# Performance work log

Measured on AMD Instinct MI355X. Metric: run time of the kernel, lower is better.

Reference implementation:

```python
import jax, jax.numpy as jnp
import numpy as np

WS = 8   # window_size
SS = 4   # shift_size
NH = 6   # num_heads
EPS = 1e-5


def _win_partition(x, ws):
    # x: [B, H, W, C] -> [B * H/ws * W/ws, ws*ws, C]
    B, H, W, C = x.shape
    x = x.reshape(B, H // ws, ws, W // ws, ws, C)
    return x.transpose(0, 1, 3, 2, 4, 5).reshape(-1, ws * ws, C)


def _win_reverse(wins, ws, H, W, B):
    C = wins.shape[-1]
    x = wins.reshape(B, H // ws, W // ws, ws, ws, C)
    return x.transpose(0, 1, 3, 2, 4, 5).reshape(B, H, W, C)


def _rel_pos_index(ws):
    # static numpy computation, identical to the torch buffer
    coords = np.stack(np.meshgrid(np.arange(ws), np.arange(ws), indexing='ij')).reshape(2, -1)
    rel = coords[:, :, None] - coords[:, None, :]          # [2, N, N]
    rel = rel.transpose(1, 2, 0).copy()                    # [N, N, 2]
    rel[..., 0] += ws - 1
    rel[..., 1] += ws - 1
    rel[..., 0] *= 2 * ws - 1
    return rel.sum(-1)                                     # [N, N] int


def _attn_mask_np(H, W, ws, ss):
    # static numpy computation of the SW-MSA mask, identical to _compute_mask
    img = np.zeros((1, H, W, 1), np.float32)
    cnt = 0
    for hs in (slice(0, -ws), slice(-ws, -ss), slice(-ss, None)):
        for wsl in (slice(0, -ws), slice(-ws, -ss), slice(-ss, None)):
            img[:, hs, wsl, :] = cnt
            cnt += 1
    mw = img.reshape(1, H // ws, ws, W // ws, ws, 1).transpose(0, 1, 3, 2, 4, 5).reshape(-1, ws * ws)
    am = mw[:, None, :] - mw[:, :, None]                   # [nW, N, N]
    return np.where(am != 0, np.float32(-100.0), np.float32(0.0))


def _swin_forward(x, qkv_w, qkv_b, proj_w, proj_b, rpb_table,
                  norm2_g, norm2_b, mlp_w1, mlp_b1, mlp_w2, mlp_b2, H, W):
    B, L, C = x.shape
    ws, ss, nh = WS, SS, NH
    hd = C // nh
    x2d = x.reshape(B, H, W, C)
    shifted = jnp.roll(x2d, (-ss, -ss), axis=(1, 2))
    win = _win_partition(shifted, ws)                      # [B_, N, C]
    B_, N, _ = win.shape

    # --- window attention (note: original applies attention to un-normalized x) ---
    qkv = (win @ qkv_w + qkv_b).reshape(B_, N, 3, nh, hd)
    q = qkv[:, :, 0].transpose(0, 2, 1, 3)                 # [B_, nh, N, hd]
    k = qkv[:, :, 1].transpose(0, 2, 1, 3)
    v = qkv[:, :, 2].transpose(0, 2, 1, 3)
    attn = jnp.einsum('bhnd,bhmd->bhnm', q, k) * (hd ** -0.5)

    bias = rpb_table[jnp.asarray(_rel_pos_index(ws)).reshape(-1)]
    bias = bias.reshape(N, N, nh).transpose(2, 0, 1)       # [nh, N, N]
    attn = attn + bias[None]

    mask = jnp.asarray(_attn_mask_np(H, W, ws, ss))        # [nW, N, N]
    nW = mask.shape[0]
    attn = attn.reshape(B_ // nW, nW, nh, N, N) + mask[None, :, None]
    attn = jax.nn.softmax(attn.reshape(B_, nh, N, N), axis=-1)

    out = jnp.einsum('bhnm,bhmd->bnhd', attn, v).reshape(B_, N, C)
    out = out @ proj_w + proj_b

    x2d = _win_reverse(out, ws, H, W, B)
    x2d = jnp.roll(x2d, (ss, ss), axis=(1, 2))
    x = x + x2d.reshape(B, L, C)

    # --- MLP branch with LayerNorm (norm2) ---
    mu = x.mean(-1, keepdims=True)
    var = x.var(-1, keepdims=True)
    xn = (x - mu) * jax.lax.rsqrt(var + EPS) * norm2_g + norm2_b
    h = jax.nn.gelu(xn @ mlp_w1 + mlp_b1, approximate=False)
    return x + (h @ mlp_w2 + mlp_b2)


def setup_inputs() -> dict:
    B, H, W, C = 8, 128, 128, 192
    mlp_hidden = 4 * C
    ks = jax.random.split(jax.random.key(0), 6)
    std = 0.02
    return {
        'x': jax.random.normal(ks[0], (B, H * W, C), jnp.float32),
        'qkv_w': jax.random.normal(ks[1], (C, 3 * C), jnp.float32) * std,
        'qkv_b': jnp.zeros((3 * C,), jnp.float32),
        'proj_w': jax.random.normal(ks[2], (C, C), jnp.float32) * std,
        'proj_b': jnp.zeros((C,), jnp.float32),
        'rpb_table': jax.random.normal(ks[3], ((2 * WS - 1) ** 2, NH), jnp.float32) * std,
        'norm2_g': jnp.ones((C,), jnp.float32),
        'norm2_b': jnp.zeros((C,), jnp.float32),
        'mlp_w1': jax.random.normal(ks[4], (C, mlp_hidden), jnp.float32) * std,
        'mlp_b1': jnp.zeros((mlp_hidden,), jnp.float32),
        'mlp_w2': jax.random.normal(ks[5], (mlp_hidden, C), jnp.float32) * std,
        'mlp_b2': jnp.zeros((C,), jnp.float32),
        'H': H,
        'W': W,
    }


def reference(x, qkv_w, qkv_b, proj_w, proj_b, rpb_table, norm2_g, norm2_b,
              mlp_w1, mlp_b1, mlp_w2, mlp_b2, H, W):
    return _swin_forward(x, qkv_w, qkv_b, proj_w, proj_b, rpb_table,
                         norm2_g, norm2_b, mlp_w1, mlp_b1, mlp_w2, mlp_b2, H, W)
```

## Files before the change

kernel.cpp:

```cpp
#include <hip/hip_runtime.h>
#include <hip/hip_bf16.h>


typedef __hip_bfloat16 bf16;
typedef __attribute__((ext_vector_type(8))) short bfrag;
typedef __attribute__((ext_vector_type(4))) float ffrag;

union bfu { bf16 h[8]; bfrag v; };

__device__ __forceinline__ float b2f(bf16 v) { return __bfloat162float(v); }
__device__ __forceinline__ bf16  f2b(float v) { return __float2bfloat16(v); }

#define MFMA(a, b, c) __builtin_amdgcn_mfma_f32_16x16x32_bf16((a), (b), (c), 0, 0, 0)

#define WS_XRES  0ULL
#define WS_OG    100663296ULL
#define WS_QKVTG 150994944ULL
#define WS_QBG   151250944ULL
#define WS_PROJT 151253504ULL
#define WS_W1T   151330304ULL
#define WS_W2T   151637504ULL
#define WS_SB    152006144ULL

__device__ __forceinline__ void stage_lds(const void* g, void* l, int nbytes, int t) {
    const int lane16 = (t & 63) * 16;
    for (int base = (t >> 6) * 1024; base < nbytes; base += 4096) {
        if (base + lane16 < nbytes) {
            __builtin_amdgcn_global_load_lds(
                (const __attribute__((address_space(1))) void*)((const char*)g + base + lane16),
                (__attribute__((address_space(3))) void*)((char*)l + base),
                16, 0, 0);
        }
    }
}

__device__ __forceinline__ float gelu_t(float x) {
    float y = x * (1.5957691216057308f + 0.07135481627f * x * x);
    return x * (1.f / (1.f + __expf(-y)));
}

__global__ __launch_bounds__(256) void k_prep(
    const float* __restrict__ qkv_w, const float* __restrict__ qkv_b,
    const float* __restrict__ proj_w, const float* __restrict__ w1,
    const float* __restrict__ w2, const float* __restrict__ rpb,
    char* __restrict__ ws)
{
    int i = blockIdx.x * 256 + threadIdx.x;
    bf16*  qkvTg = (bf16*)(ws + WS_QKVTG);
    float* qbg   = (float*)(ws + WS_QBG);
    bf16*  projT = (bf16*)(ws + WS_PROJT);
    bf16*  w1T   = (bf16*)(ws + WS_W1T);
    bf16*  w2T   = (bf16*)(ws + WS_W2T);
    bf16*  sbB   = (bf16*)(ws + WS_SB);

    if (i < 128000) {
        int g = i / 64000, rem = i % 64000;
        int c = rem / 200, k = rem % 200;
        float v = 0.f;
        if (k < 192) {
            if (c < 96)       v = qkv_w[k * 576 + g * 96 + c];
            else if (c < 192) v = qkv_w[k * 576 + 192 + g * 96 + (c - 96)];
            else if (c < 288) v = qkv_w[k * 576 + 384 + g * 96 + (c - 192)];
        }
        qkvTg[i] = f2b(v);
    } else if (i < 128640) {
        int j = i - 128000;
        int g = j / 320, c = j % 320;
        float v = 0.f;
        if (c < 96)       v = qkv_b[g * 96 + c];
        else if (c < 192) v = qkv_b[192 + g * 96 + (c - 96)];
        else if (c < 288) v = qkv_b[384 + g * 96 + (c - 192)];
        qbg[j] = v;
    } else if (i < 167040) {
        int j = i - 128640;
        int c = j / 200, k = j % 200;
        projT[j] = f2b(k < 192 ? proj_w[k * 192 + c] : 0.f);
    } else if (i < 320640) {
        int j = i - 167040;
        int c = j / 200, k = j % 200;
        w1T[j] = f2b(k < 192 ? w1[k * 768 + c] : 0.f);
    } else if (i < 504960) {
        int j = i - 320640;
        int kc = j / 7680, r = (j % 7680) / 40, kk = j % 40;
        w2T[j] = f2b(kk < 32 ? w2[(kc * 32 + kk) * 192 + r] : 0.f);
    } else if (i < 603264) {
        int j = i - 504960;
        int cls = j / 24576, h = (j % 24576) / 4096;
        int ii = (j % 4096) / 64, jj = j % 64;
        int ri = ii >> 3, ci = ii & 7, rj = jj >> 3, cj = jj & 7;
        float bias = rpb[(((ri - rj + 7) * 15) + (ci - cj + 7)) * 6 + h];
        int clsR = cls >> 1, clsC = cls & 1;
        int regi = (clsR ? (ri < 4 ? 1 : 2) : 0) * 3 + (clsC ? (ci < 4 ? 1 : 2) : 0);
        int regj = (clsR ? (rj < 4 ? 1 : 2) : 0) * 3 + (clsC ? (cj < 4 ? 1 : 2) : 0);
        sbB[j] = f2b(bias + (regi == regj ? 0.f : -100.f));
    }
}

__global__ __launch_bounds__(256, 2) void k_attn(
    const float* __restrict__ x, const char* __restrict__ ws,
    bf16* __restrict__ Og)
{
    __shared__ __align__(16) unsigned char smem[77824];
    bf16*  sWb = (bf16*)(smem);
    bf16*  sQ  = (bf16*)(smem + 25600);
    bf16*  sK  = (bf16*)(smem + 38912);
    bf16*  sVT = (bf16*)(smem + 52224);
    bf16*  sP  = (bf16*)(smem + 66048);
    float* sQB = (float*)(smem + 75264);

    const bf16*  qkvTg = (const bf16*)(ws + WS_QKVTG);
    const float* qbg   = (const float*)(ws + WS_QBG);
    const bf16*  sbB   = (const bf16*)(ws + WS_SB);

    const int t    = threadIdx.x;
    const int lane = t & 63, quad = lane >> 4, l15 = lane & 15;
    const int wave = t >> 6, r0 = wave * 16;
    const int win = blockIdx.x;
    const int b   = win >> 8;
    const int wi  = win & 255;
    const int wh  = wi >> 4, wwi = wi & 15;

    stage_lds(qbg, smem + 75264, 2560, t);
    stage_lds(qkvTg, sWb, 12800, t);

    bfrag aX[6];
    {
        int row = r0 + l15;
        int rr = row >> 3, cc = row & 7;
        int hs  = (wh * 8 + rr + 4) & 127;
        int wsx = (wwi * 8 + cc + 4) & 127;
        const float* xrow = x + ((size_t)(b * 16384 + hs * 128 + wsx)) * 192;
        #pragma unroll
        for (int kb = 0; kb < 6; kb++) {
            float4 f0 = *(const float4*)(xrow + kb * 32 + quad * 8);
            float4 f1 = *(const float4*)(xrow + kb * 32 + quad * 8 + 4);
            bfu u;
            u.h[0] = f2b(f0.x); u.h[1] = f2b(f0.y); u.h[2] = f2b(f0.z); u.h[3] = f2b(f0.w);
            u.h[4] = f2b(f1.x); u.h[5] = f2b(f1.y); u.h[6] = f2b(f1.z); u.h[7] = f2b(f1.w);
            aX[kb] = u.v;
        }
    }

    const int cls = ((wh == 15) ? 2 : 0) + ((wwi == 15) ? 1 : 0);
    const bf16* bBc = sbB + (size_t)cls * 24576;
    bf16* sPw = sP + wave * 16 * 72;

    __syncthreads();

    int pb = 0;
    for (int g = 0; g < 2; g++) {
        for (int c = 0; c < 9; c++) {
            if (c < 8)
                stage_lds(qkvTg + (size_t)(g * 320 + (c + 1) * 32) * 200,
                          sWb + (pb ^ 1) * 6400, 12800, t);
            else if (g == 0)
                stage_lds(qkvTg + (size_t)320 * 200,
                          sWb + (pb ^ 1) * 6400, 12800, t);
            const bf16* sW = sWb + pb * 6400;
            #pragma unroll
            for (int ct = 0; ct < 2; ct++) {
                int c0 = c * 32 + ct * 16;
                bfrag bw[6];
                #pragma unroll
                for (int kb = 0; kb < 6; kb++)
                    bw[kb] = *(const bfrag*)&sW[(ct * 16 + l15) * 200 + kb * 32 + quad * 8];
                ffrag acc = {0.f, 0.f, 0.f, 0.f};
                #pragma unroll
                for (int kb = 0; kb < 6; kb++) acc = MFMA(aX[kb], bw[kb], acc);
                float bias = sQB[g * 320 + c0 + l15];
                #pragma unroll
                for (int reg = 0; reg < 4; reg++) {
                    int r = r0 + quad * 4 + reg;
                    float v = acc[reg] + bias;
                    if (c0 < 96)       sQ[r * 104 + c0 + l15] = f2b(v);
                    else if (c0 < 192) sK[r * 104 + (c0 - 96) + l15] = f2b(v);
                    else               sVT[(c0 - 192 + l15) * 72 + r] = f2b(v);
                }
            }
            __syncthreads();
            pb ^= 1;
        }
        for (int hl = 0; hl < 3; hl++) {
            int h = g * 3 + hl;
            bfrag aQ = *(const bfrag*)&sQ[(r0 + l15) * 104 + hl * 32 + quad * 8];
            ffrag Sf[4];
            #pragma unroll
            for (int jt = 0; jt < 4; jt++) {
                bfrag bK = *(const bfrag*)&sK[(jt * 16 + l15) * 104 + hl * 32 + quad * 8];
                ffrag z = {0.f, 0.f, 0.f, 0.f};
                Sf[jt] = MFMA(aQ, bK, z);
            }
            const bf16* bb = bBc + h * 4096 + (r0 + quad * 4) * 64 + l15;
            #pragma unroll
            for (int jt = 0; jt < 4; jt++)
                #pragma unroll
                for (int reg = 0; reg < 4; reg++)
                    Sf[jt][reg] = Sf[jt][reg] * 0.1767766952966369f
                                + b2f(bb[reg * 64 + jt * 16]);
            #pragma unroll
            for (int reg = 0; reg < 4; reg++) {
                float m = fmaxf(fmaxf(Sf[0][reg], Sf[1][reg]), fmaxf(Sf[2][reg], Sf[3][reg]));
                m = fmaxf(m, __shfl_xor(m, 1)); m = fmaxf(m, __shfl_xor(m, 2));
                m = fmaxf(m, __shfl_xor(m, 4)); m = fmaxf(m, __shfl_xor(m, 8));
                float s = 0.f;
                #pragma unroll
                for (int jt = 0; jt < 4; jt++) { Sf[jt][reg] = __expf(Sf[jt][reg] - m); s += Sf[jt][reg]; }
                s += __shfl_xor(s, 1); s += __shfl_xor(s, 2);
                s += __shfl_xor(s, 4); s += __shfl_xor(s, 8);
                float inv = 1.f / s;
                int prow = (quad * 4 + reg) * 72;
                #pragma unroll
                for (int jt = 0; jt < 4; jt++)
                    sPw[prow + jt * 16 + l15] = f2b(Sf[jt][reg] * inv);
            }
            bfrag aP0 = *(const bfrag*)&sPw[l15 * 72 + quad * 8];
            bfrag aP1 = *(const bfrag*)&sPw[l15 * 72 + 32 + quad * 8];
            #pragma unroll
            for (int ct = 0; ct < 2; ct++) {
                bfrag bV0 = *(const bfrag*)&sVT[(hl * 32 + ct * 16 + l15) * 72 + quad * 8];
                bfrag bV1 = *(const bfrag*)&sVT[(hl * 32 + ct * 16 + l15) * 72 + 32 + quad * 8];
                ffrag z = {0.f, 0.f, 0.f, 0.f};
                ffrag o = MFMA(aP1, bV1, MFMA(aP0, bV0, z));
                #pragma unroll
                for (int reg = 0; reg < 4; reg++)
                    Og[((size_t)win * 64 + r0 + quad * 4 + reg) * 192 + h * 32 + ct * 16 + l15]
                        = f2b(o[reg]);
            }
        }
        __syncthreads();
    }
}

__global__ __launch_bounds__(256, 2) void k_proj(
    const float* __restrict__ x, const float* __restrict__ proj_b,
    const char* __restrict__ ws, float* __restrict__ xres)
{
    __shared__ __align__(16) bf16 sWp[192 * 200];

    const bf16* projT = (const bf16*)(ws + WS_PROJT);
    const bf16* Og    = (const bf16*)(ws + WS_OG);

    const int t    = threadIdx.x;
    const int lane = t & 63, quad = lane >> 4, l15 = lane & 15;
    const int wave = t >> 6, r0 = wave * 32;
    const size_t row0 = (size_t)blockIdx.x * 128;

    stage_lds(projT, sWp, 76800, t);

    bfrag aO[2][6];
    #pragma unroll
    for (int rt = 0; rt < 2; rt++)
        #pragma unroll
        for (int kb = 0; kb < 6; kb++)
            aO[rt][kb] = *(const bfrag*)&Og[(row0 + r0 + rt * 16 + l15) * 192 + kb * 32 + quad * 8];

    size_t tokb[2][4];
    #pragma unroll
    for (int rt = 0; rt < 2; rt++)
        #pragma unroll
        for (int reg = 0; reg < 4; reg++) {
            int n = r0 + rt * 16 + quad * 4 + reg;
            int w2 = (int)(blockIdx.x * 2) + (n >> 6);
            int nl = n & 63;
            int b = w2 >> 8, wi = w2 & 255;
            int wh = wi >> 4, wwi = wi & 15;
            int sr = wh * 8 + (nl >> 3), sc = wwi * 8 + (nl & 7);
            int h2 = (sr + 4) & 127, w2c = (sc + 4) & 127;
            tokb[rt][reg] = ((size_t)(b * 16384 + h2 * 128 + w2c)) * 192;
        }

    __syncthreads();

    ffrag acc[2][12];
    #pragma unroll
    for (int rt = 0; rt < 2; rt++)
        #pragma unroll
        for (int ct = 0; ct < 12; ct++)
            acc[rt][ct] = (ffrag){0.f, 0.f, 0.f, 0.f};

    #pragma unroll
    for (int ct = 0; ct < 12; ct++) {
        bfrag bw[6];
        #pragma unroll
        for (int kb = 0; kb < 6; kb++)
            bw[kb] = *(const bfrag*)&sWp[(ct * 16 + l15) * 200 + kb * 32 + quad * 8];
        #pragma unroll
        for (int rt = 0; rt < 2; rt++)
            #pragma unroll
            for (int kb = 0; kb < 6; kb++)
                acc[rt][ct] = MFMA(aO[rt][kb], bw[kb], acc[rt][ct]);
    }

    #pragma unroll
    for (int rt = 0; rt < 2; rt++)
        #pragma unroll
        for (int ct = 0; ct < 12; ct++) {
            int col = ct * 16 + l15;
            float pb = proj_b[col];
            #pragma unroll
            for (int reg = 0; reg < 4; reg++) {
                size_t gi = tokb[rt][reg] + col;
                xres[gi] = acc[rt][ct][reg] + pb + x[gi];
            }
        }
}

__global__ __launch_bounds__(256, 2) void k_mlp(
    const float* __restrict__ xres, const float* __restrict__ g,
    const float* __restrict__ bb, const float* __restrict__ b1,
    const float* __restrict__ b2, const char* __restrict__ ws,
    float* __restrict__ out)
{
    __shared__ __align__(16) unsigned char smem[69632];
    bf16*  w1base = (bf16*)(smem);
    bf16*  w2base = (bf16*)(smem + 25600);
    bf16*  hS     = (bf16*)(smem + 56320);
    float* sB1f   = (float*)(smem + 66560);
    bf16*  U      = (bf16*)(smem);

    const bf16* w1T = (const bf16*)(ws + WS_W1T);
    const bf16* w2T = (const bf16*)(ws + WS_W2T);

    const int t    = threadIdx.x;
    const int lane = t & 63, quad = lane >> 4, l15 = lane & 15;
    const int wave = t >> 6, r0 = wave * 32;
    const size_t row0 = (size_t)blockIdx.x * 128;

    stage_lds(b1, smem + 66560, 3072, t);

    #pragma unroll
    for (int p = 0; p < 2; p++) {
        int row = r0 + p * 16 + l15;
        const float4* src = (const float4*)(xres + (row0 + row) * 192 + quad * 48);
        float v[48];
        float s = 0.f, sq = 0.f;
        #pragma unroll
        for (int u = 0; u < 12; u++) {
            float4 f = src[u];
            v[u*4] = f.x; v[u*4+1] = f.y; v[u*4+2] = f.z; v[u*4+3] = f.w;
            s  += f.x + f.y + f.z + f.w;
            sq += f.x*f.x + f.y*f.y + f.z*f.z + f.w*f.w;
        }
        s  += __shfl_xor(s, 16);  s  += __shfl_xor(s, 32);
        sq += __shfl_xor(sq, 16); sq += __shfl_xor(sq, 32);
        float mean = s * (1.f / 192.f);
        float var  = sq * (1.f / 192.f) - mean * mean;
        float rstd = rsqrtf(var + 1e-5f);
        __hip_bfloat162* dst = (__hip_bfloat162*)&U[row * 200 + quad * 48];
        #pragma unroll
        for (int u = 0; u < 24; u++) {
            int c = quad * 48 + u * 2;
            float a0 = (v[u*2]   - mean) * rstd * g[c]     + bb[c];
            float a1 = (v[u*2+1] - mean) * rstd * g[c + 1] + bb[c + 1];
            dst[u] = __float22bfloat162_rn({a0, a1});
        }
    }

    bfrag aX[2][6];
    #pragma unroll
    for (int rt = 0; rt < 2; rt++)
        #pragma unroll
        for (int kb = 0; kb < 6; kb++)
            aX[rt][kb] = *(const bfrag*)&U[(r0 + rt*16 + l15) * 200 + kb*32 + quad*8];

    __syncthreads();

    stage_lds(w1T, w1base, 12800, t);
    stage_lds(w2T, w2base, 15360, t);
    __syncthreads();

    bf16* hs_w = hS + wave * 32 * 40;

    ffrag oacc[2][12];
    #pragma unroll
    for (int rt = 0; rt < 2; rt++)
        #pragma unroll
        for (int ct = 0; ct < 12; ct++)
            oacc[rt][ct] = (ffrag){0.f, 0.f, 0.f, 0.f};

    for (int kc = 0; kc < 24; kc++) {
        const int p = kc & 1;
        const bf16* w1c = w1base + p * 6400;
        const bf16* w2c = w2base + p * 7680;
        if (kc < 23) {
            stage_lds(w1T + (size_t)(kc + 1) * 6400, w1base + (p ^ 1) * 6400, 12800, t);
            stage_lds(w2T + (size_t)(kc + 1) * 7680, w2base + (p ^ 1) * 7680, 15360, t);
        }

        #pragma unroll
        for (int ct = 0; ct < 2; ct++) {
            bfrag bw[6];
            #pragma unroll
            for (int kb = 0; kb < 6; kb++)
                bw[kb] = *(const bfrag*)&w1c[(ct*16 + l15) * 200 + kb*32 + quad*8];
            float bias = sB1f[kc * 32 + ct * 16 + l15];
            #pragma unroll
            for (int rt = 0; rt < 2; rt++) {
                ffrag a = {0.f, 0.f, 0.f, 0.f};
                #pragma unroll
                for (int kb = 0; kb < 6; kb++) a = MFMA(aX[rt][kb], bw[kb], a);
                #pragma unroll
                for (int reg = 0; reg < 4; reg++)
                    hs_w[(rt*16 + quad*4 + reg) * 40 + ct*16 + l15] =
                        f2b(gelu_t(a[reg] + bias));
            }
        }
        bfrag aH[2];
        #pragma unroll
        for (int rt = 0; rt < 2; rt++)
            aH[rt] = *(const bfrag*)&hs_w[(rt*16 + l15) * 40 + quad*8];
        #pragma unroll
        for (int ct = 0; ct < 12; ct++) {
            bfrag bw2 = *(const bfrag*)&w2c[(ct*16 + l15) * 40 + quad*8];
            #pragma unroll
            for (int rt = 0; rt < 2; rt++)
                oacc[rt][ct] = MFMA(aH[rt], bw2, oacc[rt][ct]);
        }
        __syncthreads();
    }

    #pragma unroll
    for (int rt = 0; rt < 2; rt++)
        #pragma unroll
        for (int ct = 0; ct < 12; ct++) {
            int col = ct * 16 + l15;
            float b2v = b2[col];
            #pragma unroll
            for (int reg = 0; reg < 4; reg++) {
                size_t gi = (row0 + r0 + rt*16 + quad*4 + reg) * 192 + col;
                out[gi] = xres[gi] + oacc[rt][ct][reg] + b2v;
            }
        }
}

extern "C" void kernel_launch(void* const* d_in, const int* in_sizes, int n_in,
                              void* d_out, int out_size, void* d_ws, size_t ws_size,
                              hipStream_t stream)
{
    (void)in_sizes; (void)n_in; (void)out_size; (void)ws_size;

    const float* x      = (const float*)d_in[0];
    const float* qkv_w  = (const float*)d_in[1];
    const float* qkv_b  = (const float*)d_in[2];
    const float* proj_w = (const float*)d_in[3];
    const float* proj_b = (const float*)d_in[4];
    const float* rpb    = (const float*)d_in[5];
    const float* n2g    = (const float*)d_in[6];
    const float* n2b    = (const float*)d_in[7];
    const float* w1     = (const float*)d_in[8];
    const float* b1     = (const float*)d_in[9];
    const float* w2     = (const float*)d_in[10];
    const float* b2     = (const float*)d_in[11];

    char*  ws   = (char*)d_ws;
    float* xres = (float*)(ws + WS_XRES);
    bf16*  Og   = (bf16*)(ws + WS_OG);
    float* out  = (float*)d_out;

    hipLaunchKernelGGL(k_prep, dim3(2357), dim3(256), 0, stream,
                       qkv_w, qkv_b, proj_w, w1, w2, rpb, ws);
    hipLaunchKernelGGL(k_attn, dim3(2048), dim3(256), 0, stream,
                       x, ws, Og);
    hipLaunchKernelGGL(k_proj, dim3(1024), dim3(256), 0, stream,
                       x, proj_b, ws, xres);
    hipLaunchKernelGGL(k_mlp,  dim3(1024), dim3(256), 0, stream,
                       xres, n2g, n2b, b1, b2, ws, out);
}
```

Before: 482.8 us.

## Halve MLP block tile and drop weight double-buffering to raise occupancy

The MLP kernel now processes 64 rows per block instead of 128, giving each wave a single 16-row tile. It also replaces the double-buffered weight staging with a single buffer that is reloaded after a barrier. Together these cut shared memory and register use so launch bounds can ask for four blocks per CU, and the grid doubles to 2048 blocks. The cost is that every block re-streams the full W1/W2 weights for half the rows, doubling weight traffic, and the copy-compute overlap inside a block is lost, which now relies on other resident blocks to hide it.

```diff
diff --git a/kernel.cpp b/kernel.cpp
--- a/kernel.cpp
+++ b/kernel.cpp
@@ -305,32 +305,31 @@
         }
 }
 
-__global__ __launch_bounds__(256, 2) void k_mlp(
+__global__ __launch_bounds__(256, 4) void k_mlp(
     const float* __restrict__ xres, const float* __restrict__ g,
     const float* __restrict__ bb, const float* __restrict__ b1,
     const float* __restrict__ b2, const char* __restrict__ ws,
     float* __restrict__ out)
 {
-    __shared__ __align__(16) unsigned char smem[69632];
-    bf16*  w1base = (bf16*)(smem);
-    bf16*  w2base = (bf16*)(smem + 25600);
-    bf16*  hS     = (bf16*)(smem + 56320);
-    float* sB1f   = (float*)(smem + 66560);
-    bf16*  U      = (bf16*)(smem);
+    __shared__ __align__(16) unsigned char smem[36352];
+    bf16*  w1s  = (bf16*)(smem);
+    bf16*  w2s  = (bf16*)(smem + 12800);
+    bf16*  hS   = (bf16*)(smem + 28160);
+    float* sB1f = (float*)(smem + 33280);
+    bf16*  U    = (bf16*)(smem);
 
     const bf16* w1T = (const bf16*)(ws + WS_W1T);
     const bf16* w2T = (const bf16*)(ws + WS_W2T);
 
     const int t    = threadIdx.x;
     const int lane = t & 63, quad = lane >> 4, l15 = lane & 15;
-    const int wave = t >> 6, r0 = wave * 32;
-    const size_t row0 = (size_t)blockIdx.x * 128;
-
-    stage_lds(b1, smem + 66560, 3072, t);
-
-    #pragma unroll
-    for (int p = 0; p < 2; p++) {
-        int row = r0 + p * 16 + l15;
+    const int wave = t >> 6, r0 = wave * 16;
+    const size_t row0 = (size_t)blockIdx.x * 64;
+
+    stage_lds(b1, smem + 33280, 3072, t);
+
+    {
+        int row = r0 + l15;
         const float4* src = (const float4*)(xres + (row0 + row) * 192 + quad * 48);
         float v[48];
         float s = 0.f, sq = 0.f;
@@ -355,82 +354,66 @@
             dst[u] = __float22bfloat162_rn({a0, a1});
         }
     }
-
-    bfrag aX[2][6];
-    #pragma unroll
-    for (int rt = 0; rt < 2; rt++)
-        #pragma unroll
-        for (int kb = 0; kb < 6; kb++)
-            aX[rt][kb] = *(const bfrag*)&U[(r0 + rt*16 + l15) * 200 + kb*32 + quad*8];
-
     __syncthreads();
 
-    stage_lds(w1T, w1base, 12800, t);
-    stage_lds(w2T, w2base, 15360, t);
+    bfrag aX[6];
+    #pragma unroll
+    for (int kb = 0; kb < 6; kb++)
+        aX[kb] = *(const bfrag*)&U[(r0 + l15) * 200 + kb*32 + quad*8];
+
     __syncthreads();
 
-    bf16* hs_w = hS + wave * 32 * 40;
-
-    ffrag oacc[2][12];
-    #pragma unroll
-    for (int rt = 0; rt < 2; rt++)
-        #pragma unroll
-        for (int ct = 0; ct < 12; ct++)
-            oacc[rt][ct] = (ffrag){0.f, 0.f, 0.f, 0.f};
+    stage_lds(w1T, w1s, 12800, t);
+    stage_lds(w2T, (char*)w2s, 15360, t);
+    __syncthreads();
+
+    bf16* hs_w = hS + wave * 16 * 40;
+
+    ffrag oacc[12];
+    #pragma unroll
+    for (int ct = 0; ct < 12; ct++)
+        oacc[ct] = (ffrag){0.f, 0.f, 0.f, 0.f};
 
     for (int kc = 0; kc < 24; kc++) {
-        const int p = kc & 1;
-        const bf16* w1c = w1base + p * 6400;
-        const bf16* w2c = w2base + p * 7680;
-        if (kc < 23) {
-            stage_lds(w1T + (size_t)(kc + 1) * 6400, w1base + (p ^ 1) * 6400, 12800, t);
-            stage_lds(w2T + (size_t)(kc + 1) * 7680, w2base + (p ^ 1) * 7680, 15360, t);
-        }
-
         #pragma unroll
         for (int ct = 0; ct < 2; ct++) {
             bfrag bw[6];
             #pragma unroll
             for (int kb = 0; kb < 6; kb++)
-                bw[kb] = *(const bfrag*)&w1c[(ct*16 + l15) * 200 + kb*32 + quad*8];
+                bw[kb] = *(const bfrag*)&w1s[(ct*16 + l15) * 200 + kb*32 + quad*8];
             float bias = sB1f[kc * 32 + ct * 16 + l15];
-            #pragma unroll
-            for (int rt = 0; rt < 2; rt++) {
-                ffrag a = {0.f, 0.f, 0.f, 0.f};
-                #pragma unroll
-                for (int kb = 0; kb < 6; kb++) a = MFMA(aX[rt][kb], bw[kb], a);
-                #pragma unroll
-                for (int reg = 0; reg < 4; reg++)
-                    hs_w[(rt*16 + quad*4 + reg) * 40 + ct*16 + l15] =
-                        f2b(gelu_t(a[reg] + bias));
-            }
-        }
-        bfrag aH[2];
-        #pragma unroll
-        for (int rt = 0; rt < 2; rt++)
-            aH[rt] = *(const bfrag*)&hs_w[(rt*16 + l15) * 40 + quad*8];
+            ffrag a = {0.f, 0.f, 0.f, 0.f};
+            #pragma unroll
+            for (int kb = 0; kb < 6; kb++) a = MFMA(aX[kb], bw[kb], a);
+            #pragma unroll
+            for (int reg = 0; reg < 4; reg++)
+                hs_w[(quad*4 + reg) * 40 + ct*16 + l15] =
+                    f2b(gelu_t(a[reg] + bias));
+        }
+        bfrag aH = *(const bfrag*)&hs_w[l15 * 40 + quad*8];
         #pragma unroll
         for (int ct = 0; ct < 12; ct++) {
-            bfrag bw2 = *(const bfrag*)&w2c[(ct*16 + l15) * 40 + quad*8];
-            #pragma unroll
-            for (int rt = 0; rt < 2; rt++)
-                oacc[rt][ct] = MFMA(aH[rt], bw2, oacc[rt][ct]);
+            bfrag bw2 = *(const bfrag*)&w2s[(ct*16 + l15) * 40 + quad*8];
+            oacc[ct] = MFMA(aH, bw2, oacc[ct]);
         }
         __syncthreads();
-    }
-
-    #pragma unroll
-    for (int rt = 0; rt < 2; rt++)
-        #pragma unroll
-        for (int ct = 0; ct < 12; ct++) {
-            int col = ct * 16 + l15;
-            float b2v = b2[col];
-            #pragma unroll
-            for (int reg = 0; reg < 4; reg++) {
-                size_t gi = (row0 + r0 + rt*16 + quad*4 + reg) * 192 + col;
-                out[gi] = xres[gi] + oacc[rt][ct][reg] + b2v;
-            }
-        }
+        if (kc < 23) {
+            stage_lds(w1T + (size_t)(kc + 1) * 6400, w1s, 12800, t);
+            stage_lds(w2T + (size_t)(kc + 1) * 7680, (char*)w2s, 15360, t);
+            __syncthreads();
+        }
+    }
+
+    #pragma unroll
+    for (int ct = 0; ct < 12; ct++) {
+        int col = ct * 16 + l15;
+        float b2v = b2[col];
+        #pragma unroll
+        for (int reg = 0; reg < 4; reg++) {
+            size_t gi = (row0 + r0 + quad*4 + reg) * 192 + col;
+            out[gi] = xres[gi] + oacc[ct][reg] + b2v;
+        }
+    }
 }
 
 extern "C" void kernel_launch(void* const* d_in, const int* in_sizes, int n_in,
@@ -463,6 +446,6 @@
                        x, ws, Og);
     hipLaunchKernelGGL(k_proj, dim3(1024), dim3(256), 0, stream,
                        x, proj_b, ws, xres);
-    hipLaunchKernelGGL(k_mlp,  dim3(1024), dim3(256), 0, stream,
+    hipLaunchKernelGGL(k_mlp,  dim3(2048), dim3(256), 0, stream,
                        xres, n2g, n2b, b1, b2, ws, out);
 }
```

Result: no change. 479.6 us (-0.7%).
